# Optimization experiments

Measured on AMD Instinct MI355X. Metric: run time of the kernel, lower is better.

## Reference

```python
import jax, jax.numpy as jnp
import numpy as np
from jax import lax

B, H, W = 16, 64, 64
CHANNELS = 512
N_BLOCKS, CIN_B, COUT_B = 16, 32, 32
K = 3  # kernel size, 'same' padding, stride 1


def setup_inputs() -> dict:
    key = jax.random.key(0)
    k1, k2, k3, k4, k5 = jax.random.split(key, 5)
    x = jax.random.normal(k1, (B, H, W, CHANNELS), dtype=jnp.float32)
    # per-block conv kernels, HWIO per block: [n_blocks, kh, kw, cin_b, cout_b]
    fan_in = K * K * CIN_B
    weights = jax.random.normal(k2, (N_BLOCKS, K, K, CIN_B, COUT_B), dtype=jnp.float32) / np.sqrt(fan_in)
    bias = jax.random.normal(k3, (CHANNELS,), dtype=jnp.float32) * 0.05
    # disjoint channel partitions (realistic block routing); gather may duplicate, scatter sums
    blocks_in = jax.random.permutation(k4, CHANNELS).reshape(N_BLOCKS, CIN_B).astype(jnp.int32)
    blocks_out = jax.random.permutation(k5, CHANNELS).reshape(N_BLOCKS, COUT_B).astype(jnp.int32)
    return {"x": x, "weights": weights, "bias": bias,
            "blocks_in": blocks_in, "blocks_out": blocks_out}


def reference(x, weights, bias, blocks_in, blocks_out):
    n_blocks, cin_b = blocks_in.shape
    cout_b = blocks_out.shape[1]
    # gather: [B,H,W, n_blocks*cin_b], grouped channel layout
    xg = x[..., blocks_in.reshape(-1)]
    # grouped-conv kernel HWIO: I=cin_b per group, O = n_blocks*cout_b (groups along O)
    kernel = jnp.transpose(weights, (1, 2, 3, 0, 4)).reshape(K, K, cin_b, n_blocks * cout_b)
    y = lax.conv_general_dilated(
        xg, kernel, window_strides=(1, 1), padding='SAME',
        dimension_numbers=('NHWC', 'HWIO', 'NHWC'),
        feature_group_count=n_blocks)  # [B,H,W, n_blocks*cout_b]
    # scatter_nd semantics: duplicates accumulate
    out = jnp.zeros((x.shape[0], y.shape[1], y.shape[2], CHANNELS), dtype=y.dtype)
    out = out.at[..., blocks_out.reshape(-1)].add(y)
    out = out + bias
    return jax.nn.relu(out)
```

## Files before the change

kernel.cpp:

```cpp
#include <hip/hip_runtime.h>

#define NSLOT 4
#define SLOT_B 18432
#define OROW_OFF (NSLOT*SLOT_B)
#define SMEM2 (OROW_OFF + 2*16*512*4)

typedef __attribute__((ext_vector_type(8))) short bf16x8;
typedef __attribute__((ext_vector_type(4))) float f32x4;
typedef __attribute__((ext_vector_type(4))) unsigned int u32x4;

__device__ __forceinline__ short f2bf(float f) {
  union { float f; unsigned u; } v; v.f = f;
  unsigned r = v.u + 0x7FFFu + ((v.u >> 16) & 1u);
  return (short)(r >> 16);
}

__device__ __forceinline__ void gld_lds16(const void* g, void* l) {
  __builtin_amdgcn_global_load_lds(
      (__attribute__((address_space(1))) void*)(g),
      (__attribute__((address_space(3))) void*)(l), 16, 0, 0);
}

__global__ __launch_bounds__(256) void permute_kernel(
    const float* __restrict__ x, const int* __restrict__ bin,
    unsigned char* __restrict__ xs)
{
  __shared__ unsigned short pos_tab[512];
  __shared__ char stage[4][1024];
  const int t = threadIdx.x;
  { int c0 = bin[t], c1 = bin[t + 256];
    pos_tab[c0] = (unsigned short)t; pos_tab[c1] = (unsigned short)(t + 256); }
  __syncthreads();

  const int w = t >> 6, lane = t & 63;
  char* st = stage[w];
  const int pbase = blockIdx.x * 32 + w * 8;
  for (int i = 0; i < 8; ++i) {
    const int p = pbase + i;
    const unsigned swz = (unsigned)((((p & 63) + 1) & 7) << 4);
    const float* src = x + (size_t)p * 512 + lane * 4;
    f32x4 v0 = *(const f32x4*)(src);
    f32x4 v1 = *(const f32x4*)(src + 256);
    const int cb = lane * 4;
#pragma unroll
    for (int k = 0; k < 4; ++k)
      *(short*)(st + (((unsigned)pos_tab[cb + k] * 2u) ^ swz)) = f2bf(v0[k]);
#pragma unroll
    for (int k = 0; k < 4; ++k)
      *(short*)(st + (((unsigned)pos_tab[256 + cb + k] * 2u) ^ swz)) = f2bf(v1[k]);
    asm volatile("s_waitcnt lgkmcnt(0)" ::: "memory");
    u32x4 d = *(const u32x4*)(st + lane * 16);
    *(u32x4*)(xs + (size_t)p * 1024 + lane * 16) = d;
  }
}

__global__ __launch_bounds__(1024, 4) void conv_kernel(
    const unsigned char* __restrict__ xs, const float* __restrict__ wts,
    const float* __restrict__ bias, const int* __restrict__ bout,
    float* __restrict__ out)
{
  extern __shared__ char smem[];
  float* orow = (float*)(smem + OROW_OFF);

  const int t = threadIdx.x;
  const int lane = t & 63;
  const int g = t >> 6;
  const int g4 = lane >> 4;
  const int n16 = lane & 15;

  const int bid = blockIdx.x;
  const int b = bid >> 4;
  const int strip = (bid >> 2) & 3;
  const int seg = bid & 3;
  const int hs = seg * 16;
  const int w0 = strip * 16;

  {
    u32x4 z = {0, 0, 0, 0};
    for (int zz = t; zz < (NSLOT * SLOT_B) / 16; zz += 1024)
      *(u32x4*)(smem + zz * 16) = z;
  }

  bf16x8 wf[9][2];
  {
    const float* Wg = wts + g * (9 * 32 * 32);
#pragma unroll
    for (int tap = 0; tap < 9; ++tap)
#pragma unroll
      for (int nt = 0; nt < 2; ++nt) {
        bf16x8 f;
#pragma unroll
        for (int j = 0; j < 8; ++j)
          f[j] = f2bf(Wg[(tap * 32 + g4 * 8 + j) * 32 + nt * 16 + n16]);
        wf[tap][nt] = f;
      }
  }
  const int opos0 = bout[g * 32 + n16];
  const int opos1 = bout[g * 32 + 16 + n16];
  const int c4 = (t & 127) << 2;
  const int pixq = t >> 7;
  const f32x4 bias4 = *(const f32x4*)(bias + c4);

  auto stage_row = [&](int grow) {
    if (grow < 0 || grow > 63) return;
    char* slot = smem + (grow & 3) * SLOT_B;
    const unsigned char* src = xs + ((size_t)((b * 64 + grow) * 64 + (w0 - 1)) * 1024);
    int gcol0 = w0 - 1 + g;
    if (gcol0 >= 0)
      gld_lds16(src + g * 1024 + lane * 16, slot + g * 1024);
    if (g < 2) {
      int c = g + 16;
      if (w0 - 1 + c < 64)
        gld_lds16(src + c * 1024 + lane * 16, slot + c * 1024);
    }
  };

  __syncthreads();
  stage_row(hs - 1); stage_row(hs); stage_row(hs + 1);
  __syncthreads();

  const int gbase = g * 64 + g4 * 16;
  const size_t outb = (size_t)b * (64 * 64 * 512);
  const int hstage_max = (hs + 16 < 63) ? hs + 16 : 63;

  for (int h = hs; h < hs + 16; ++h) {
    if (h + 2 <= hstage_max) {
      stage_row(h + 2);
    } else if (h + 2 == 64) {
      u32x4 z = {0, 0, 0, 0};
      *(u32x4*)(smem + t * 16) = z;
      if (t < 128) *(u32x4*)(smem + 16384 + t * 16) = z;
    }

    if (h > hs) {
      const float* ob = orow + ((h - 1) & 1) * 8192;
#pragma unroll
      for (int s = 0; s < 2; ++s) {
        int pix = pixq + s * 8;
        f32x4 y = *(const f32x4*)(ob + pix * 512 + c4);
        f32x4 o;
        o[0] = fmaxf(y[0] + bias4[0], 0.f);
        o[1] = fmaxf(y[1] + bias4[1], 0.f);
        o[2] = fmaxf(y[2] + bias4[2], 0.f);
        o[3] = fmaxf(y[3] + bias4[3], 0.f);
        *(f32x4*)(out + outb + (size_t)((h - 1) * 64 + w0 + pix) * 512 + c4) = o;
      }
    }

    f32x4 a0 = {0, 0, 0, 0}, a1 = {0, 0, 0, 0};
#pragma unroll
    for (int dh = 0; dh < 3; ++dh) {
      const char* sb = smem + ((h - 1 + dh) & 3) * SLOT_B;
#pragma unroll
      for (int dw = 0; dw < 3; ++dw) {
        int col = n16 + dw;
        int addr = (col * 1024 + gbase) ^ ((col & 7) << 4);
        bf16x8 a = *(const bf16x8*)(sb + addr);
        a0 = __builtin_amdgcn_mfma_f32_16x16x32_bf16(a, wf[dh * 3 + dw][0], a0, 0, 0, 0);
        a1 = __builtin_amdgcn_mfma_f32_16x16x32_bf16(a, wf[dh * 3 + dw][1], a1, 0, 0, 0);
      }
    }

    float* oh = orow + (h & 1) * 8192;
#pragma unroll
    for (int rr = 0; rr < 4; ++rr) {
      int m = (g4 * 4 + rr) * 512;
      oh[m + opos0] = a0[rr];
      oh[m + opos1] = a1[rr];
    }
    __syncthreads();
  }

  {
    const int h1 = hs + 15;
    const float* ob = orow + (h1 & 1) * 8192;
#pragma unroll
    for (int s = 0; s < 2; ++s) {
      int pix = pixq + s * 8;
      f32x4 y = *(const f32x4*)(ob + pix * 512 + c4);
      f32x4 o;
      o[0] = fmaxf(y[0] + bias4[0], 0.f);
      o[1] = fmaxf(y[1] + bias4[1], 0.f);
      o[2] = fmaxf(y[2] + bias4[2], 0.f);
      o[3] = fmaxf(y[3] + bias4[3], 0.f);
      *(f32x4*)(out + outb + (size_t)(h1 * 64 + w0 + pix) * 512 + c4) = o;
    }
  }
}

extern "C" void kernel_launch(void* const* d_in, const int* in_sizes, int n_in,
                              void* d_out, int out_size, void* d_ws, size_t ws_size,
                              hipStream_t stream) {
  const float* x    = (const float*)d_in[0];
  const float* wts  = (const float*)d_in[1];
  const float* bias = (const float*)d_in[2];
  const int*   bin  = (const int*)d_in[3];
  const int*   bout = (const int*)d_in[4];
  float* out = (float*)d_out;
  unsigned char* xs = (unsigned char*)d_ws;
  (void)in_sizes; (void)n_in; (void)out_size; (void)ws_size;

  permute_kernel<<<dim3(2048), dim3(256), 0, stream>>>(x, bin, xs);
  conv_kernel<<<dim3(256), dim3(1024), SMEM2, stream>>>(xs, wts, bias, bout, out);
}
```

Baseline: 131.5 us.

## Retile conv to 4x4 pixel patches with 16-row LDS ring and swizzled epilogue

The conv kernel now gives each block a 4-column strip over all 64 rows and computes a 4x4 pixel patch per MFMA step. Inputs stream into a 16-row LDS ring with deeper prefetch and hand-placed waitcnt/barriers in place of __syncthreads. The output tile is single-buffered and XOR-swizzled to cut bank conflicts, and each lane writes 8 contiguous channels. The permute kernel's pixel order and swizzle are changed to match the new LDS layout. Halo reuse per block changes, and the single output buffer adds a barrier per step.

```diff
diff --git a/kernel.cpp b/kernel.cpp
--- a/kernel.cpp
+++ b/kernel.cpp
@@ -1,9 +1,7 @@
 #include <hip/hip_runtime.h>
 
-#define NSLOT 4
-#define SLOT_B 18432
-#define OROW_OFF (NSLOT*SLOT_B)
-#define SMEM2 (OROW_OFF + 2*16*512*4)
+#define RING_B (16*6144)
+#define SMEM2  (RING_B + 16*512*4)
 
 typedef __attribute__((ext_vector_type(8))) short bf16x8;
 typedef __attribute__((ext_vector_type(4))) float f32x4;
@@ -26,29 +24,37 @@
     unsigned char* __restrict__ xs)
 {
   __shared__ unsigned short pos_tab[512];
-  __shared__ char stage[4][1024];
+  __shared__ char stage[4][2][1024];
   const int t = threadIdx.x;
-  { int c0 = bin[t], c1 = bin[t + 256];
-    pos_tab[c0] = (unsigned short)t; pos_tab[c1] = (unsigned short)(t + 256); }
+  { int cA = bin[t], cB = bin[t + 256];
+    pos_tab[cA] = (unsigned short)t;
+    pos_tab[cB] = (unsigned short)(t + 256); }
   __syncthreads();
 
   const int w = t >> 6, lane = t & 63;
-  char* st = stage[w];
-  const int pbase = blockIdx.x * 32 + w * 8;
-  for (int i = 0; i < 8; ++i) {
-    const int p = pbase + i;
-    const unsigned swz = (unsigned)((((p & 63) + 1) & 7) << 4);
-    const float* src = x + (size_t)p * 512 + lane * 4;
-    f32x4 v0 = *(const f32x4*)(src);
+  const int q = blockIdx.x;
+  const int i = q & 255, sub = q >> 8;
+  const int b = i >> 4, strip = i & 15;
+  const int cb = lane * 4;
+
+#pragma unroll 2
+  for (int k = 0; k < 8; ++k) {
+    const int idx = w * 8 + k;
+    const int r  = sub * 8 + (idx >> 2);
+    const int gc = strip * 4 + (idx & 3);
+    const int p  = (b * 64 + r) * 64 + gc;
+    const unsigned swz = ((unsigned)((r & 3) | ((gc & 1) << 2))) << 4;
+    const float* src = x + (size_t)p * 512 + cb;
+    f32x4 v0 = *(const f32x4*)src;
     f32x4 v1 = *(const f32x4*)(src + 256);
-    const int cb = lane * 4;
+    char* st = stage[w][k & 1];
 #pragma unroll
-    for (int k = 0; k < 4; ++k)
-      *(short*)(st + (((unsigned)pos_tab[cb + k] * 2u) ^ swz)) = f2bf(v0[k]);
+    for (int j = 0; j < 4; ++j)
+      *(short*)(st + ((pos_tab[cb + j] * 2u) ^ swz)) = f2bf(v0[j]);
 #pragma unroll
-    for (int k = 0; k < 4; ++k)
-      *(short*)(st + (((unsigned)pos_tab[256 + cb + k] * 2u) ^ swz)) = f2bf(v1[k]);
-    asm volatile("s_waitcnt lgkmcnt(0)" ::: "memory");
+    for (int j = 0; j < 4; ++j)
+      *(short*)(st + ((pos_tab[256 + cb + j] * 2u) ^ swz)) = f2bf(v1[j]);
+    asm volatile("s_waitcnt lgkmcnt(0)");
     u32x4 d = *(const u32x4*)(st + lane * 16);
     *(u32x4*)(xs + (size_t)p * 1024 + lane * 16) = d;
   }
@@ -60,30 +66,22 @@
     float* __restrict__ out)
 {
   extern __shared__ char smem[];
-  float* orow = (float*)(smem + OROW_OFF);
+  float* orow = (float*)(smem + RING_B);
 
-  const int t = threadIdx.x;
-  const int lane = t & 63;
-  const int g = t >> 6;
-  const int g4 = lane >> 4;
-  const int n16 = lane & 15;
+  const int t = threadIdx.x, lane = t & 63, g = t >> 6;
+  const int g4 = lane >> 4, n16 = lane & 15;
+  const int bid = blockIdx.x;
+  const int b = bid >> 4, strip = bid & 15;
+  const int w0 = strip * 4;
+  const int gbase = g * 64 + g4 * 16;
 
-  const int bid = blockIdx.x;
-  const int b = bid >> 4;
-  const int strip = (bid >> 2) & 3;
-  const int seg = bid & 3;
-  const int hs = seg * 16;
-  const int w0 = strip * 16;
-
-  {
-    u32x4 z = {0, 0, 0, 0};
-    for (int zz = t; zz < (NSLOT * SLOT_B) / 16; zz += 1024)
-      *(u32x4*)(smem + zz * 16) = z;
-  }
+  u32x4 z4 = {0, 0, 0, 0};
+  for (int zz = t * 16; zz < RING_B; zz += 16384)
+    *(u32x4*)(smem + zz) = z4;
 
   bf16x8 wf[9][2];
   {
-    const float* Wg = wts + g * (9 * 32 * 32);
+    const float* Wg = wts + g * 9216;
 #pragma unroll
     for (int tap = 0; tap < 9; ++tap)
 #pragma unroll
@@ -95,96 +93,83 @@
         wf[tap][nt] = f;
       }
   }
-  const int opos0 = bout[g * 32 + n16];
-  const int opos1 = bout[g * 32 + 16 + n16];
-  const int c4 = (t & 127) << 2;
-  const int pixq = t >> 7;
-  const f32x4 bias4 = *(const f32x4*)(bias + c4);
+  const int opos0x = bout[g * 32 + n16] ^ (g4 << 2);
+  const int opos1x = bout[g * 32 + 16 + n16] ^ (g4 << 2);
 
-  auto stage_row = [&](int grow) {
-    if (grow < 0 || grow > 63) return;
-    char* slot = smem + (grow & 3) * SLOT_B;
-    const unsigned char* src = xs + ((size_t)((b * 64 + grow) * 64 + (w0 - 1)) * 1024);
-    int gcol0 = w0 - 1 + g;
-    if (gcol0 >= 0)
-      gld_lds16(src + g * 1024 + lane * 16, slot + g * 1024);
-    if (g < 2) {
-      int c = g + 16;
-      if (w0 - 1 + c < 64)
-        gld_lds16(src + c * 1024 + lane * 16, slot + c * 1024);
-    }
-  };
+  const int c8 = lane * 8;
+  const f32x4 b0 = *(const f32x4*)(bias + c8);
+  const f32x4 b1 = *(const f32x4*)(bias + c8 + 4);
+  const int fp = g, fg4 = g >> 2;
+  const int fq0 = fp * 2048 + ((((lane * 2) + 0) ^ fg4) << 4);
+  const int fq1 = fp * 2048 + ((((lane * 2) + 1) ^ fg4) << 4);
+  const size_t pixbase = (size_t)((b * 64 + (fp >> 2)) * 64 + w0 + (fp & 3)) * 512 + c8;
+
+  const int r0 = g / 6,        c0 = g - r0 * 6;
+  const int r1 = (g + 16) / 6, c1 = (g + 16) - r1 * 6;
+  const int gc0 = w0 - 1 + c0, gc1 = w0 - 1 + c1;
+  const bool cv0 = (gc0 >= 0 && gc0 <= 63);
+  const bool cv1 = (gc1 >= 0 && gc1 <= 63);
+  const unsigned char* xb = xs + (size_t)(b * 64) * 64 * 1024;
 
   __syncthreads();
-  stage_row(hs - 1); stage_row(hs); stage_row(hs + 1);
-  __syncthreads();
+  if (cv0) gld_lds16(xb + (size_t)(r0 * 64 + gc0) * 1024 + lane * 16,
+                     smem + r0 * 6144 + c0 * 1024);
+  if (g < 14 && cv1) gld_lds16(xb + (size_t)(r1 * 64 + gc1) * 1024 + lane * 16,
+                               smem + r1 * 6144 + c1 * 1024);
+  asm volatile("s_waitcnt vmcnt(0)\ns_barrier" ::: "memory");
 
-  const int gbase = g * 64 + g4 * 16;
-  const size_t outb = (size_t)b * (64 * 64 * 512);
-  const int hstage_max = (hs + 16 < 63) ? hs + 16 : 63;
-
-  for (int h = hs; h < hs + 16; ++h) {
-    if (h + 2 <= hstage_max) {
-      stage_row(h + 2);
-    } else if (h + 2 == 64) {
-      u32x4 z = {0, 0, 0, 0};
-      *(u32x4*)(smem + t * 16) = z;
-      if (t < 128) *(u32x4*)(smem + 16384 + t * 16) = z;
+  for (int h = 0; h < 64; h += 4) {
+    {
+      int gr0 = h + 5 + r0;
+      if (gr0 <= 63 && cv0)
+        gld_lds16(xb + (size_t)(gr0 * 64 + gc0) * 1024 + lane * 16,
+                  smem + (gr0 & 15) * 6144 + c0 * 1024);
+      int gr1 = h + 5 + r1;
+      if (g < 8 && gr1 <= 63 && cv1)
+        gld_lds16(xb + (size_t)(gr1 * 64 + gc1) * 1024 + lane * 16,
+                  smem + (gr1 & 15) * 6144 + c1 * 1024);
+      if (h == 56 && t < 384) *(u32x4*)(smem + t * 16) = z4;
     }
-
-    if (h > hs) {
-      const float* ob = orow + ((h - 1) & 1) * 8192;
-#pragma unroll
-      for (int s = 0; s < 2; ++s) {
-        int pix = pixq + s * 8;
-        f32x4 y = *(const f32x4*)(ob + pix * 512 + c4);
-        f32x4 o;
-        o[0] = fmaxf(y[0] + bias4[0], 0.f);
-        o[1] = fmaxf(y[1] + bias4[1], 0.f);
-        o[2] = fmaxf(y[2] + bias4[2], 0.f);
-        o[3] = fmaxf(y[3] + bias4[3], 0.f);
-        *(f32x4*)(out + outb + (size_t)((h - 1) * 64 + w0 + pix) * 512 + c4) = o;
-      }
-    }
+    asm volatile("" ::: "memory");
 
     f32x4 a0 = {0, 0, 0, 0}, a1 = {0, 0, 0, 0};
 #pragma unroll
     for (int dh = 0; dh < 3; ++dh) {
-      const char* sb = smem + ((h - 1 + dh) & 3) * SLOT_B;
+      int gr = h + (n16 >> 2) + dh - 1;
+      int rowbase = (gr & 15) * 6144;
+      int rsw = (gr & 3) << 4;
 #pragma unroll
       for (int dw = 0; dw < 3; ++dw) {
-        int col = n16 + dw;
-        int addr = (col * 1024 + gbase) ^ ((col & 7) << 4);
-        bf16x8 a = *(const bf16x8*)(sb + addr);
+        int cs = (n16 & 3) + dw;
+        int csw = ((w0 - 1 + cs) & 1) << 6;
+        const char* ap = smem + rowbase + cs * 1024 + (gbase ^ rsw ^ csw);
+        bf16x8 a = *(const bf16x8*)ap;
         a0 = __builtin_amdgcn_mfma_f32_16x16x32_bf16(a, wf[dh * 3 + dw][0], a0, 0, 0, 0);
         a1 = __builtin_amdgcn_mfma_f32_16x16x32_bf16(a, wf[dh * 3 + dw][1], a1, 0, 0, 0);
       }
     }
 
-    float* oh = orow + (h & 1) * 8192;
 #pragma unroll
     for (int rr = 0; rr < 4; ++rr) {
-      int m = (g4 * 4 + rr) * 512;
-      oh[m + opos0] = a0[rr];
-      oh[m + opos1] = a1[rr];
+      float* oh = orow + (g4 * 4 + rr) * 512;
+      oh[opos0x] = a0[rr];
+      oh[opos1x] = a1[rr];
     }
-    __syncthreads();
-  }
+    asm volatile("s_waitcnt lgkmcnt(0)\ns_barrier" ::: "memory");
 
-  {
-    const int h1 = hs + 15;
-    const float* ob = orow + (h1 & 1) * 8192;
-#pragma unroll
-    for (int s = 0; s < 2; ++s) {
-      int pix = pixq + s * 8;
-      f32x4 y = *(const f32x4*)(ob + pix * 512 + c4);
-      f32x4 o;
-      o[0] = fmaxf(y[0] + bias4[0], 0.f);
-      o[1] = fmaxf(y[1] + bias4[1], 0.f);
-      o[2] = fmaxf(y[2] + bias4[2], 0.f);
-      o[3] = fmaxf(y[3] + bias4[3], 0.f);
-      *(f32x4*)(out + outb + (size_t)(h1 * 64 + w0 + pix) * 512 + c4) = o;
+    {
+      f32x4 y0 = *(const f32x4*)((const char*)orow + fq0);
+      f32x4 y1 = *(const f32x4*)((const char*)orow + fq1);
+      f32x4 o0, o1;
+      o0[0] = fmaxf(y0[0] + b0[0], 0.f); o0[1] = fmaxf(y0[1] + b0[1], 0.f);
+      o0[2] = fmaxf(y0[2] + b0[2], 0.f); o0[3] = fmaxf(y0[3] + b0[3], 0.f);
+      o1[0] = fmaxf(y1[0] + b1[0], 0.f); o1[1] = fmaxf(y1[1] + b1[1], 0.f);
+      o1[2] = fmaxf(y1[2] + b1[2], 0.f); o1[3] = fmaxf(y1[3] + b1[3], 0.f);
+      float* dst = out + pixbase + (size_t)h * 32768;
+      *(f32x4*)dst = o0;
+      *(f32x4*)(dst + 4) = o1;
     }
+    asm volatile("s_waitcnt vmcnt(2) lgkmcnt(0)\ns_barrier" ::: "memory");
   }
 }
 
```

Measured after the change: 143.3 us. 1.09x slower.
